# Optimization experiments

Hardware: AMD Instinct MI355X
Metric: run time of the kernel (lower is better)

Reference implementation:

```python
import jax, jax.numpy as jnp
import numpy as np

H = 512      # hidden_size
OUT = 1      # output_size (forced by prev_output shape (B,1,1))
B = 64       # batch
T = 1024     # output_length


def setup_inputs() -> dict:
    key = jax.random.key(0)
    ks = jax.random.split(key, 10)
    s_in = 1.0 / np.sqrt(H)
    return {
        "context_vector": jax.random.normal(ks[0], (B, 1, H), jnp.float32),
        "expected_output": jax.random.normal(ks[1], (B, T, OUT), jnp.float32),
        "W_ih0": jax.random.normal(ks[2], (3 * H, H + OUT), jnp.float32) * s_in,
        "W_hh0": jax.random.normal(ks[3], (3 * H, H), jnp.float32) * s_in,
        "b_ih0": jnp.zeros((3 * H,), jnp.float32),
        "b_hh0": jnp.zeros((3 * H,), jnp.float32),
        "W_ih1": jax.random.normal(ks[4], (3 * H, H), jnp.float32) * s_in,
        "W_hh1": jax.random.normal(ks[5], (3 * H, H), jnp.float32) * s_in,
        "b_ih1": jnp.zeros((3 * H,), jnp.float32),
        "b_hh1": jnp.zeros((3 * H,), jnp.float32),
        "W_o1": jax.random.normal(ks[6], (H, H), jnp.float32) * s_in,
        "b_o1": jnp.zeros((H,), jnp.float32),
        "W_o2": jax.random.normal(ks[7], (OUT, H), jnp.float32) * s_in,
        "b_o2": jnp.zeros((OUT,), jnp.float32),
        "force": 0,  # teacher forcing disabled (original uses python random -> nondeterministic)
    }


def _gru_cell(x, h, W_ih, W_hh, b_ih, b_hh):
    # PyTorch GRU cell math
    gi = x @ W_ih.T + b_ih          # (B, 3H)
    gh = h @ W_hh.T + b_hh          # (B, 3H)
    i_r, i_z, i_n = jnp.split(gi, 3, axis=-1)
    h_r, h_z, h_n = jnp.split(gh, 3, axis=-1)
    r = jax.nn.sigmoid(i_r + h_r)
    z = jax.nn.sigmoid(i_z + h_z)
    n = jnp.tanh(i_n + r * h_n)
    return (1.0 - z) * n + z * h


def reference(context_vector, expected_output, W_ih0, W_hh0, b_ih0, b_hh0,
              W_ih1, W_hh1, b_ih1, b_hh1, W_o1, b_o1, W_o2, b_o2, force):
    del force  # force=False path only (deterministic)
    batch = context_vector.shape[0]
    out_len = expected_output.shape[1]
    ctx = context_vector[:, 0, :]                      # (B, H)
    h0 = jnp.zeros((batch, H), context_vector.dtype)
    h1 = jnp.zeros((batch, H), context_vector.dtype)
    prev = jnp.zeros((batch, OUT), context_vector.dtype)

    def step(carry, _):
        h0, h1, prev = carry
        x = jnp.concatenate([ctx, prev], axis=1)       # (B, H+1)
        h0n = _gru_cell(x, h0, W_ih0, W_hh0, b_ih0, b_hh0)
        h1n = _gru_cell(h0n, h1, W_ih1, W_hh1, b_ih1, b_hh1)
        y = jax.nn.relu(h1n @ W_o1.T + b_o1)           # (B, H)
        y = jax.nn.relu(y @ W_o2.T + b_o2)             # (B, 1)
        return (h0n, h1n, y), y

    (h0, h1, _), ys = jax.lax.scan(step, (h0, h1, prev), None, length=out_len)
    outputs = jnp.transpose(ys, (1, 0, 2))             # (B, T, 1)
    h_i = jnp.stack([h0, h1], axis=0)                  # (n_layers, B, H)
    return outputs, h_i
```

## Files before the change

### kernel.cpp

```cpp
#include <hip/hip_runtime.h>
#include <stdint.h>


#define NWG 256
#define NT  256
#define TT  1024

typedef unsigned short ushort;
typedef unsigned int   uint;
typedef __attribute__((ext_vector_type(8))) short short8;
typedef __attribute__((ext_vector_type(4))) float f32x4;
typedef __attribute__((ext_vector_type(4))) uint  uint4v;

struct __align__(16) SmemR0 {
  ushort wpl[2][48*520];
  float  gictx[3*16*68];
  float  wcol[3][16];
  float  bhnN[16];
  float  prevS[64];
};
struct __align__(16) SmemR2 {
  ushort whh[2][48*520];
  ushort wih[48*520];
  float  xk[3][64][16];
  float  bsumR[16], bsumZ[16], binN[16], bhnN[16];
};
struct __align__(16) SmemR3 {
  ushort wpl[2][16*520];
  float  xk[2][64][4];
  float  bo1v[16], wo2v[16];
};

__device__ __forceinline__ float frcp(float x){
#if __has_builtin(__builtin_amdgcn_rcpf)
  return __builtin_amdgcn_rcpf(x);
#else
  return 1.f/x;
#endif
}
__device__ __forceinline__ float sigm(float x){ return frcp(1.f + __expf(-x)); }
__device__ __forceinline__ float tanh_f(float x){
  return 1.f - 2.f*frcp(__expf(2.f*x) + 1.f);
}
__device__ __forceinline__ float bf2f(ushort h){ return __uint_as_float(((uint)h)<<16); }
__device__ __forceinline__ ushort bfrnd(float x){
  uint u = __float_as_uint(x);
  return (ushort)((u + 0x7fffu + ((u>>16)&1u)) >> 16);
}
#define SWP(p, v)  (void)__hip_atomic_exchange((uint*)(p), (uint)(v), __ATOMIC_RELAXED, __HIP_MEMORY_SCOPE_AGENT)
#define ALD1(p)    __hip_atomic_load((const uint*)(p), __ATOMIC_RELAXED, __HIP_MEMORY_SCOPE_AGENT)
#define ALDF(p)    __uint_as_float(ALD1(p))
#define FADDI(p)   (void)__hip_atomic_fetch_add((p), 1, __ATOMIC_RELAXED, __HIP_MEMORY_SCOPE_AGENT)

__device__ __forceinline__ void gbar(int* slots, int* epoch, int w, int tid, int e){
  __syncthreads();
  if (tid == 0)
    __hip_atomic_store(&slots[w], e, __ATOMIC_RELEASE, __HIP_MEMORY_SCOPE_AGENT);
  if (w == 0 && tid < 64){
    for(;;){
      int m0 = __hip_atomic_load(&slots[tid*4+0], __ATOMIC_RELAXED, __HIP_MEMORY_SCOPE_AGENT);
      int m1 = __hip_atomic_load(&slots[tid*4+1], __ATOMIC_RELAXED, __HIP_MEMORY_SCOPE_AGENT);
      int m2 = __hip_atomic_load(&slots[tid*4+2], __ATOMIC_RELAXED, __HIP_MEMORY_SCOPE_AGENT);
      int m3 = __hip_atomic_load(&slots[tid*4+3], __ATOMIC_RELAXED, __HIP_MEMORY_SCOPE_AGENT);
      if (__all(min(min(m0,m1),min(m2,m3)) >= e)) break;
      __builtin_amdgcn_s_sleep(1);
    }
    if (tid == 0){
      __builtin_amdgcn_fence(__ATOMIC_ACQUIRE, "agent");
      __hip_atomic_store(epoch, e, __ATOMIC_RELEASE, __HIP_MEMORY_SCOPE_AGENT);
    }
  }
  if (tid == 0){
    while (__hip_atomic_load(epoch, __ATOMIC_RELAXED, __HIP_MEMORY_SCOPE_AGENT) < e)
      __builtin_amdgcn_s_sleep(1);
    __builtin_amdgcn_fence(__ATOMIC_ACQUIRE, "agent");
  }
  __syncthreads();
}

__device__ __forceinline__ void drain_sync(){
  __builtin_amdgcn_s_waitcnt(0);
  __syncthreads();
}
__device__ __forceinline__ void waitmail(const int* w, int target, int tid){
  if (tid == 0)
    while ((int)ALD1(w) < target) {}
  __syncthreads();
}
__device__ __forceinline__ void waitmail2(const int* a, const int* b, int target, int tid){
  if (tid == 0)
    while ((int)ALD1(a) < target || (int)ALD1(b) < target) {}
  __syncthreads();
}

#define LD1SCD(dst, addr) \
  asm volatile("global_load_dword %0, %1, off sc0 sc1" : "=v"(dst) : "v"(addr));
#define STSH(addr, val) \
  asm volatile("global_store_short %0, %1, off sc0 sc1" :: "v"(addr), "v"(val) : "memory");
#define ST4SC(addr, val) \
  asm volatile("global_store_dwordx4 %0, %1, off sc0 sc1" :: "v"(addr), "v"(val) : "memory");
#define LD4A(DST, P, OFS) \
  asm volatile("global_load_dwordx4 %0, %1, off sc0 sc1" : "=v"(DST) : "v"((P) + (OFS)));
#define VMBAR4(a,b,c,d) \
  asm volatile("s_waitcnt vmcnt(0)" : "+v"(a),"+v"(b),"+v"(c),"+v"(d));
#define VMBAR8(a,b,c,d,e,f,g,h) \
  asm volatile("s_waitcnt vmcnt(0)" \
               : "+v"(a),"+v"(b),"+v"(c),"+v"(d),"+v"(e),"+v"(f),"+v"(g),"+v"(h));

#define MFMA_ __builtin_amdgcn_mfma_f32_16x16x32_bf16

#define DECL_HILO(PH, PL) \
  uint4v ha0,ha1,ha2,ha3,ha4,ha5,ha6,ha7,ha8,ha9,ha10,ha11,ha12,ha13,ha14,ha15; \
  uint4v la0,la1,la2,la3,la4,la5,la6,la7,la8,la9,la10,la11,la12,la13,la14,la15; \
  LD4A(ha0,PH,aoffB+0*32) LD4A(ha1,PH,aoffB+1*32) LD4A(ha2,PH,aoffB+2*32) LD4A(ha3,PH,aoffB+3*32) \
  LD4A(ha4,PH,aoffB+4*32) LD4A(ha5,PH,aoffB+5*32) LD4A(ha6,PH,aoffB+6*32) LD4A(ha7,PH,aoffB+7*32) \
  LD4A(ha8,PH,aoffB+8*32) LD4A(ha9,PH,aoffB+9*32) LD4A(ha10,PH,aoffB+10*32) LD4A(ha11,PH,aoffB+11*32) \
  LD4A(ha12,PH,aoffB+12*32) LD4A(ha13,PH,aoffB+13*32) LD4A(ha14,PH,aoffB+14*32) LD4A(ha15,PH,aoffB+15*32) \
  LD4A(la0,PL,aoffB+0*32) LD4A(la1,PL,aoffB+1*32) LD4A(la2,PL,aoffB+2*32) LD4A(la3,PL,aoffB+3*32) \
  LD4A(la4,PL,aoffB+4*32) LD4A(la5,PL,aoffB+5*32) LD4A(la6,PL,aoffB+6*32) LD4A(la7,PL,aoffB+7*32) \
  LD4A(la8,PL,aoffB+8*32) LD4A(la9,PL,aoffB+9*32) LD4A(la10,PL,aoffB+10*32) LD4A(la11,PL,aoffB+11*32) \
  LD4A(la12,PL,aoffB+12*32) LD4A(la13,PL,aoffB+13*32) LD4A(la14,PL,aoffB+14*32) LD4A(la15,PL,aoffB+15*32) \
  VMBAR8(ha0,ha1,ha2,ha3,ha4,ha5,ha6,ha7) \
  VMBAR8(ha8,ha9,ha10,ha11,ha12,ha13,ha14,ha15) \
  VMBAR8(la0,la1,la2,la3,la4,la5,la6,la7) \
  VMBAR8(la8,la9,la10,la11,la12,la13,la14,la15)

#define MS3F(i) { \
  short8 AH_ = __builtin_bit_cast(short8, ha##i); \
  short8 AL_ = __builtin_bit_cast(short8, la##i); \
  const int ko_ = (i)*32 + q*8; \
  short8 bh_ = *(const short8*)(&S0.wpl[0][(col)*520 + ko_]); \
  short8 bl_ = *(const short8*)(&S0.wpl[1][(col)*520 + ko_]); \
  acc0 = MFMA_(AH_, bh_, acc0, 0,0,0); \
  acc0 = MFMA_(AL_, bh_, acc0, 0,0,0); \
  acc0 = MFMA_(AH_, bl_, acc0, 0,0,0); \
  bh_ = *(const short8*)(&S0.wpl[0][(16+col)*520 + ko_]); \
  bl_ = *(const short8*)(&S0.wpl[1][(16+col)*520 + ko_]); \
  acc1 = MFMA_(AH_, bh_, acc1, 0,0,0); \
  acc1 = MFMA_(AL_, bh_, acc1, 0,0,0); \
  acc1 = MFMA_(AH_, bl_, acc1, 0,0,0); \
  bh_ = *(const short8*)(&S0.wpl[0][(32+col)*520 + ko_]); \
  bl_ = *(const short8*)(&S0.wpl[1][(32+col)*520 + ko_]); \
  acc2 = MFMA_(AH_, bh_, acc2, 0,0,0); \
  acc2 = MFMA_(AL_, bh_, acc2, 0,0,0); \
  acc2 = MFMA_(AH_, bl_, acc2, 0,0,0); }

#define GH1(i) { \
  short8 AH_ = __builtin_bit_cast(short8, ha##i); \
  short8 AL_ = __builtin_bit_cast(short8, la##i); \
  const int ko_ = kq + (i)*32 + q*8; \
  short8 bh_ = *(const short8*)(&S2.whh[0][(col)*520 + ko_]); \
  short8 bl_ = *(const short8*)(&S2.whh[1][(col)*520 + ko_]); \
  aR = MFMA_(AH_, bh_, aR, 0,0,0); \
  aR = MFMA_(AL_, bh_, aR, 0,0,0); \
  aR = MFMA_(AH_, bl_, aR, 0,0,0); \
  bh_ = *(const short8*)(&S2.whh[0][(16+col)*520 + ko_]); \
  bl_ = *(const short8*)(&S2.whh[1][(16+col)*520 + ko_]); \
  aZ = MFMA_(AH_, bh_, aZ, 0,0,0); \
  aZ = MFMA_(AL_, bh_, aZ, 0,0,0); \
  aZ = MFMA_(AH_, bl_, aZ, 0,0,0); \
  bh_ = *(const short8*)(&S2.whh[0][(32+col)*520 + ko_]); \
  bl_ = *(const short8*)(&S2.whh[1][(32+col)*520 + ko_]); \
  aNh = MFMA_(AH_, bh_, aNh, 0,0,0); \
  aNh = MFMA_(AL_, bh_, aNh, 0,0,0); \
  aNh = MFMA_(AH_, bl_, aNh, 0,0,0); }

#define GI1(i) { \
  short8 AH_ = __builtin_bit_cast(short8, ga##i); \
  const int ko_ = kq + (i)*32 + q*8; \
  short8 bh_ = *(const short8*)(&S2.wih[(col)*520 + ko_]); \
  aR = MFMA_(AH_, bh_, aR, 0,0,0); \
  bh_ = *(const short8*)(&S2.wih[(16+col)*520 + ko_]); \
  aZ = MFMA_(AH_, bh_, aZ, 0,0,0); \
  bh_ = *(const short8*)(&S2.wih[(32+col)*520 + ko_]); \
  aNi = MFMA_(AH_, bh_, aNi, 0,0,0); }

#define DECL_HI8(P) \
  uint4v ha0,ha1,ha2,ha3,ha4,ha5,ha6,ha7; \
  LD4A(ha0,P,aoff8+0*32) LD4A(ha1,P,aoff8+1*32) LD4A(ha2,P,aoff8+2*32) LD4A(ha3,P,aoff8+3*32) \
  LD4A(ha4,P,aoff8+4*32) LD4A(ha5,P,aoff8+5*32) LD4A(ha6,P,aoff8+6*32) LD4A(ha7,P,aoff8+7*32) \
  VMBAR8(ha0,ha1,ha2,ha3,ha4,ha5,ha6,ha7)

#define MS1H(i) { \
  short8 AH_ = __builtin_bit_cast(short8, ha##i); \
  const int ko_ = kb + (i)*32 + q*8; \
  short8 bh_ = *(const short8*)(&S3.wpl[0][(col)*520 + ko_]); \
  short8 bl_ = *(const short8*)(&S3.wpl[1][(col)*520 + ko_]); \
  acc0 = MFMA_(AH_, bh_, acc0, 0,0,0); \
  acc0 = MFMA_(AH_, bl_, acc0, 0,0,0); }

#define RUN16(M) M(0) M(1) M(2) M(3) M(4) M(5) M(6) M(7) \
                 M(8) M(9) M(10) M(11) M(12) M(13) M(14) M(15)
#define RUN8(M)  M(0) M(1) M(2) M(3) M(4) M(5) M(6) M(7)
#define RUN4(M)  M(0) M(1) M(2) M(3)

extern "C" __global__ void __launch_bounds__(NT, 1)
decoder_rnn(const float* __restrict__ ctx,
            const float* __restrict__ Wih0,
            const float* __restrict__ Whh0,
            const float* __restrict__ bih0,
            const float* __restrict__ bhh0g,
            const float* __restrict__ Wih1,
            const float* __restrict__ Whh1,
            const float* __restrict__ bih1g,
            const float* __restrict__ bhh1g,
            const float* __restrict__ Wo1,
            const float* __restrict__ bo1g,
            const float* __restrict__ Wo2,
            const float* __restrict__ bo2g,
            float* __restrict__ out,
            float* __restrict__ ws)
{
  extern __shared__ char smem_raw[];
  SmemR0& S0 = *reinterpret_cast<SmemR0*>(smem_raw);
  SmemR2& S2 = *reinterpret_cast<SmemR2*>(smem_raw);
  SmemR3& S3 = *reinterpret_cast<SmemR3*>(smem_raw);
  const int tid = threadIdx.x;
  const int wg  = blockIdx.x;

  ushort* hp  = (ushort*)ws;
  float* yout = (float*)ws + 196608;
  int*  ibase = (int*)((float*)ws + 200704);
  int* gslots = ibase;
  int* epoch  = ibase + 256;
  int* mbox   = ibase + 512;

  const float bo2v = bo2g[0];

  for (int i = wg*NT + tid; i < 200704; i += NWG*NT)
    SWP((uint*)ws + i, 0u);
  if (wg == 0)
    for (int i = tid; i < 256*32; i += NT) SWP(mbox + i, 0);

  const int gid   = wg >> 7;
  const int m     = wg & 127;
  const int bbase = 32*gid;
  int role, j, bh = 0;
  if (m < 32){ role = 0; j = m; }
  else if (m < 96){ role = 2; bh = (m - 32) >> 5; j = m & 31; }
  else { role = 3; j = m - 96; }

  if (role == 0){
    for (int i = tid; i < 48*512; i += NT){
      int r = i >> 9, k = i & 511;
      int g3 = r >> 4, n = r & 15;
      float wv = Whh0[(size_t)(g3*512 + 16*j + n)*512 + k];
      ushort hh = bfrnd(wv);
      S0.wpl[0][r*520 + k] = hh;
      S0.wpl[1][r*520 + k] = bfrnd(wv - bf2f(hh));
    }
    if (tid < 48){
      int g3 = tid >> 4, n = tid & 15;
      S0.wcol[g3][n] = Wih0[(size_t)(g3*512 + 16*j + n)*513 + 512];
    }
    if (tid < 16) S0.bhnN[tid] = bhh0g[2*512 + 16*j + tid];
    for (int idx = tid; idx < 1536; idx += NT){
      int r = idx >> 5, bl = idx & 31;
      int g3 = r >> 4, n = r & 15;
      int grow = g3*512 + 16*j + n;
      const float* wr = Wih0 + (size_t)grow*513;
      const float* cx = ctx  + (size_t)(bbase + bl)*512;
      float s = bih0[grow];
      if (g3 < 2) s += bhh0g[grow];
      #pragma unroll 4
      for (int k = 0; k < 512; ++k) s += wr[k]*cx[k];
      S0.gictx[g3*1088 + n*68 + bl] = s;
    }
  } else if (role == 2){
    for (int i = tid; i < 48*512; i += NT){
      int r = i >> 9, k = i & 511;
      int g3 = r >> 4, n = r & 15;
      size_t row = (size_t)(g3*512 + 16*j + n)*512 + k;
      float wv = Whh1[row];
      ushort hh = bfrnd(wv);
      S2.whh[0][r*520 + k] = hh;
      S2.whh[1][r*520 + k] = bfrnd(wv - bf2f(hh));
      S2.wih[r*520 + k] = bfrnd(Wih1[row]);
    }
    if (tid < 16){
      int n = tid;
      S2.bsumR[n] = bih1g[16*j + n]       + bhh1g[16*j + n];
      S2.bsumZ[n] = bih1g[512 + 16*j + n] + bhh1g[512 + 16*j + n];
      S2.binN[n]  = bih1g[1024 + 16*j + n];
      S2.bhnN[n]  = bhh1g[1024 + 16*j + n];
    }
  } else {
    for (int i = tid; i < 16*512; i += NT){
      int r = i >> 9, k = i & 511;
      float wv = Wo1[(size_t)(16*j + r)*512 + k];
      ushort hh = bfrnd(wv);
      S3.wpl[0][r*520 + k] = hh;
      S3.wpl[1][r*520 + k] = bfrnd(wv - bf2f(hh));
    }
    if (tid < 16){ S3.bo1v[tid] = bo1g[16*j + tid]; S3.wo2v[tid] = Wo2[16*j + tid]; }
  }

  gbar(gslots, epoch, wg, tid, 1);

  int* myline = mbox + wg*32;
  const int gb = gid*128;

  const int v   = tid >> 6;
  const int l   = tid & 63;
  const int q   = l >> 4;
  const int col = l & 15;
  const int ng  = 16*j + col;

  if (role == 0){
    const int bblk  = v & 1;
    const int aoffB = (bbase + 16*bblk + col)*512 + q*8;
    const int b0wL  = 16*bblk + 4*q;
    float hc0 = 0.f, hc1 = 0.f, hc2 = 0.f, hc3 = 0.f;
    for (int t = 0; t < TT; ++t){
      const int r0 = t & 1, w0 = r0 ^ 1;
      waitmail(myline + 0, 32*t, tid);
      const ushort* rH = hp + r0*32768;
      const ushort* rL = hp + 65536 + r0*32768;
      ushort*       wH = hp + w0*32768;
      ushort*       wL = hp + 65536 + w0*32768;
      f32x4 acc0={0,0,0,0}, acc1={0,0,0,0}, acc2={0,0,0,0};
      if (v < 2){
        DECL_HILO(rH, rL)
        RUN16(MS3F)
      }
      waitmail(myline + 1, 32*t, tid);
      if (tid < 32){
        float s = 0.f;
        if (t > 0){
          const float* yp = yout + ((t-1)&1)*2048 + bbase + tid;
          float vv[32];
          #pragma unroll
          for (int jj = 0; jj < 32; ++jj)
            LD1SCD(vv[jj], yp + jj*64)
          VMBAR8(vv[0],vv[1],vv[2],vv[3],vv[4],vv[5],vv[6],vv[7])
          VMBAR8(vv[8],vv[9],vv[10],vv[11],vv[12],vv[13],vv[14],vv[15])
          VMBAR8(vv[16],vv[17],vv[18],vv[19],vv[20],vv[21],vv[22],vv[23])
          VMBAR8(vv[24],vv[25],vv[26],vv[27],vv[28],vv[29],vv[30],vv[31])
          #pragma unroll
          for (int jj = 0; jj < 32; ++jj) s += vv[jj];
        }
        float pv = fmaxf(s + bo2v, 0.f);
        S0.prevS[tid] = pv;
        if (j == 0 && t > 0) out[(size_t)(bbase + tid)*TT + (t-1)] = pv;
      }
      __syncthreads();
      if (v < 2){
        f32x4 pv4 = *(const f32x4*)&S0.prevS[b0wL];
        f32x4 gR = *(const f32x4*)&S0.gictx[0*1088 + col*68 + b0wL];
        f32x4 gZ = *(const f32x4*)&S0.gictx[1*1088 + col*68 + b0wL];
        f32x4 gN = *(const f32x4*)&S0.gictx[2*1088 + col*68 + b0wL];
        float wc0 = S0.wcol[0][col], wc1 = S0.wcol[1][col], wc2 = S0.wcol[2][col];
        float bhn = S0.bhnN[col];
        #define E0(i, HC) { \
          float rr = sigm(gR[i] + pv4[i]*wc0 + acc0[i]); \
          float zz = sigm(gZ[i] + pv4[i]*wc1 + acc1[i]); \
          float nn = tanh_f(gN[i] + pv4[i]*wc2 + rr*(acc2[i] + bhn)); \
          float h = (1.f-zz)*nn + zz*HC; \
          HC = h; \
          ushort hh_ = bfrnd(h); \
          uint hu_ = hh_, lu_ = bfrnd(h - bf2f(hh_)); \
          STSH(wH + (size_t)(bbase + b0wL + (i))*512 + ng, hu_) \
          STSH(wL + (size_t)(bbase + b0wL + (i))*512 + ng, lu_) }
        E0(0,hc0) E0(1,hc1) E0(2,hc2) E0(3,hc3)
        #undef E0
      }
      drain_sync();
      if (tid < 96)
        FADDI(mbox + (gb + tid)*32 + 0);
    }
  } else if (role == 2){
    ushort* p1H = hp + 131072;
    ushort* p1L = hp + 163840;
    const int bb16  = bbase + 16*bh;
    const int kq    = v*128;
    const int aoffA = (bb16 + col)*512 + kq + q*8;
    float hc0 = 0.f, hc1 = 0.f, hc2 = 0.f, hc3 = 0.f;
    for (int t = 0; t < TT; ++t){
      const int w0 = (t & 1) ^ 1;
      waitmail(myline + 1 + bh, 32*t, tid);
      f32x4 aR={0,0,0,0}, aZ={0,0,0,0}, aNi={0,0,0,0}, aNh={0,0,0,0};
      {
        uint4v ha0,ha1,ha2,ha3, la0,la1,la2,la3;
        LD4A(ha0, p1H, aoffA+0*32) LD4A(ha1, p1H, aoffA+1*32)
        LD4A(ha2, p1H, aoffA+2*32) LD4A(ha3, p1H, aoffA+3*32)
        LD4A(la0, p1L, aoffA+0*32) LD4A(la1, p1L, aoffA+1*32)
        LD4A(la2, p1L, aoffA+2*32) LD4A(la3, p1L, aoffA+3*32)
        VMBAR8(ha0,ha1,ha2,ha3,la0,la1,la2,la3)
        RUN4(GH1)
      }
      waitmail(myline + 0, 32*(t+1), tid);
      {
        const ushort* rH = hp + w0*32768;
        uint4v ga0,ga1,ga2,ga3;
        LD4A(ga0, rH, aoffA+0*32) LD4A(ga1, rH, aoffA+1*32)
        LD4A(ga2, rH, aoffA+2*32) LD4A(ga3, rH, aoffA+3*32)
        VMBAR4(ga0,ga1,ga2,ga3)
        RUN4(GI1)
      }
      if (v >= 1){
        *(f32x4*)&S2.xk[v-1][l][0]  = aR;
        *(f32x4*)&S2.xk[v-1][l][4]  = aZ;
        *(f32x4*)&S2.xk[v-1][l][8]  = aNi;
        *(f32x4*)&S2.xk[v-1][l][12] = aNh;
      }
      __syncthreads();
      if (v == 0){
        #pragma unroll
        for (int w = 0; w < 3; ++w){
          aR  += *(const f32x4*)&S2.xk[w][l][0];
          aZ  += *(const f32x4*)&S2.xk[w][l][4];
          aNi += *(const f32x4*)&S2.xk[w][l][8];
          aNh += *(const f32x4*)&S2.xk[w][l][12];
        }
        float bsR = S2.bsumR[col], bsZ = S2.bsumZ[col];
        float biN = S2.binN[col],  bhN = S2.bhnN[col];
        #define E1(i, HC) { \
          float r1 = sigm(aR[i] + bsR); \
          float z1 = sigm(aZ[i] + bsZ); \
          float n1 = tanh_f(aNi[i] + biN + r1*(aNh[i] + bhN)); \
          float h = (1.f-z1)*n1 + z1*HC; \
          HC = h; \
          ushort hh_ = bfrnd(h); \
          uint hu_ = hh_, lu_ = bfrnd(h - bf2f(hh_)); \
          STSH(p1H + (size_t)(bb16 + 4*q + (i))*512 + ng, hu_) \
          STSH(p1L + (size_t)(bb16 + 4*q + (i))*512 + ng, lu_) }
        E1(0,hc0) E1(1,hc1) E1(2,hc2) E1(3,hc3)
        #undef E1
      }
      drain_sync();
      if (tid < 96)
        FADDI(mbox + (gb + 32 + tid)*32 + 1 + bh);
    }
  } else {
    const ushort* rH = hp + 131072;
    const int bblk  = v & 1;
    const int kb    = (v >> 1)*256;
    const int aoff8 = (bbase + 16*bblk + col)*512 + kb + q*8;
    const int b0wL  = 16*bblk + 4*q;
    for (int t = 0; t < TT; ++t){
      waitmail2(myline + 1, myline + 2, 32*(t+1), tid);
      f32x4 acc0={0,0,0,0};
      {
        DECL_HI8(rH)
        RUN8(MS1H)
      }
      if (v >= 2)
        *(f32x4*)&S3.xk[bblk][l][0] = acc0;
      __syncthreads();
      if (v < 2){
        acc0 += *(const f32x4*)&S3.xk[bblk][l][0];
        float s0 = S3.wo2v[col]*fmaxf(acc0[0] + S3.bo1v[col], 0.f);
        float s1 = S3.wo2v[col]*fmaxf(acc0[1] + S3.bo1v[col], 0.f);
        float s2 = S3.wo2v[col]*fmaxf(acc0[2] + S3.bo1v[col], 0.f);
        float s3 = S3.wo2v[col]*fmaxf(acc0[3] + S3.bo1v[col], 0.f);
        #pragma unroll
        for (int d = 1; d < 16; d <<= 1){
          s0 += __shfl_xor(s0, d);
          s1 += __shfl_xor(s1, d);
          s2 += __shfl_xor(s2, d);
          s3 += __shfl_xor(s3, d);
        }
        if (col == 0){
          float* rp = yout + (t&1)*2048 + j*64 + bbase + b0wL;
          f32x4 sv = {s0, s1, s2, s3};
          ST4SC(rp, sv)
        }
      }
      drain_sync();
      if (tid < 32)
        FADDI(mbox + (gb + tid)*32 + 1);
    }
  }

  gbar(gslots, epoch, wg, tid, 2);
  if (wg == 0 && tid < 64){
    float s = 0.f;
    const float* yp = yout + 2048 + tid;
    #pragma unroll
    for (int jj = 0; jj < 32; ++jj) s += ALDF(yp + jj*64);
    out[(size_t)tid*TT + 1023] = fmaxf(s + bo2v, 0.f);
  }
  {
    int g = wg*256 + tid;
    if (g < 32768) out[65536 + g] = bf2f(hp[g]) + bf2f(hp[65536 + g]);
    else {
      int g2 = g - 32768;
      out[65536 + g] = bf2f(hp[131072 + g2]) + bf2f(hp[163840 + g2]);
    }
  }
}

extern "C" void kernel_launch(void* const* d_in, const int* in_sizes, int n_in,
                              void* d_out, int out_size, void* d_ws, size_t ws_size,
                              hipStream_t stream){
  const float* ctx   = (const float*)d_in[0];
  const float* Wih0  = (const float*)d_in[2];
  const float* Whh0  = (const float*)d_in[3];
  const float* bih0  = (const float*)d_in[4];
  const float* bhh0  = (const float*)d_in[5];
  const float* Wih1  = (const float*)d_in[6];
  const float* Whh1  = (const float*)d_in[7];
  const float* bih1  = (const float*)d_in[8];
  const float* bhh1  = (const float*)d_in[9];
  const float* Wo1   = (const float*)d_in[10];
  const float* bo1   = (const float*)d_in[11];
  const float* Wo2   = (const float*)d_in[12];
  const float* bo2   = (const float*)d_in[13];

  (void)in_sizes; (void)n_in; (void)out_size; (void)ws_size;

  const int smem_sz = (int)sizeof(SmemR2);
  (void)hipFuncSetAttribute((const void*)decoder_rnn,
                            hipFuncAttributeMaxDynamicSharedMemorySize,
                            smem_sz);

  decoder_rnn<<<NWG, NT, smem_sz, stream>>>(
      ctx, Wih0, Whh0, bih0, bhh0, Wih1, Whh1, bih1, bhh1,
      Wo1, bo1, Wo2, bo2, (float*)d_out, (float*)d_ws);
}
```

Before: 8.770 ms.

## Replace atomic-counter mailboxes with per-producer flag slots polled as vector loads

Each producer workgroup now writes its step number into its own dword slot in a wider mailbox line, instead of atomically incrementing a shared counter. Consumers poll the whole 32-slot line with eight dwordx4 loads and take the minimum. The aim is to avoid contention from many fetch_add atomics hitting the same address on every timestep. The mailbox area triples in size, and polling now issues more load traffic per iteration. The prev-output sum also changes from a serial loop to a tree reduction.

```diff
diff --git a/kernel.cpp b/kernel.cpp
--- a/kernel.cpp
+++ b/kernel.cpp
@@ -50,7 +50,6 @@
 #define SWP(p, v)  (void)__hip_atomic_exchange((uint*)(p), (uint)(v), __ATOMIC_RELAXED, __HIP_MEMORY_SCOPE_AGENT)
 #define ALD1(p)    __hip_atomic_load((const uint*)(p), __ATOMIC_RELAXED, __HIP_MEMORY_SCOPE_AGENT)
 #define ALDF(p)    __uint_as_float(ALD1(p))
-#define FADDI(p)   (void)__hip_atomic_fetch_add((p), 1, __ATOMIC_RELAXED, __HIP_MEMORY_SCOPE_AGENT)
 
 __device__ __forceinline__ void gbar(int* slots, int* epoch, int w, int tid, int e){
   __syncthreads();
@@ -82,21 +81,13 @@
   __builtin_amdgcn_s_waitcnt(0);
   __syncthreads();
 }
-__device__ __forceinline__ void waitmail(const int* w, int target, int tid){
-  if (tid == 0)
-    while ((int)ALD1(w) < target) {}
-  __syncthreads();
-}
-__device__ __forceinline__ void waitmail2(const int* a, const int* b, int target, int tid){
-  if (tid == 0)
-    while ((int)ALD1(a) < target || (int)ALD1(b) < target) {}
-  __syncthreads();
-}
 
 #define LD1SCD(dst, addr) \
   asm volatile("global_load_dword %0, %1, off sc0 sc1" : "=v"(dst) : "v"(addr));
 #define STSH(addr, val) \
   asm volatile("global_store_short %0, %1, off sc0 sc1" :: "v"(addr), "v"(val) : "memory");
+#define STI(addr, val) \
+  asm volatile("global_store_dword %0, %1, off sc0 sc1" :: "v"(addr), "v"(val) : "memory");
 #define ST4SC(addr, val) \
   asm volatile("global_store_dwordx4 %0, %1, off sc0 sc1" :: "v"(addr), "v"(val) : "memory");
 #define LD4A(DST, P, OFS) \
@@ -106,6 +97,47 @@
 #define VMBAR8(a,b,c,d,e,f,g,h) \
   asm volatile("s_waitcnt vmcnt(0)" \
                : "+v"(a),"+v"(b),"+v"(c),"+v"(d),"+v"(e),"+v"(f),"+v"(g),"+v"(h));
+
+__device__ __forceinline__ int min4i(uint4v a){
+  return min(min((int)a.x,(int)a.y), min((int)a.z,(int)a.w));
+}
+__device__ __forceinline__ void waitline(const int* line, int target, int tid){
+  if (tid == 0){
+    const uint* p = (const uint*)line;
+    for(;;){
+      uint4v a0,a1,a2,a3,a4,a5,a6,a7;
+      LD4A(a0,p,0)  LD4A(a1,p,4)  LD4A(a2,p,8)  LD4A(a3,p,12)
+      LD4A(a4,p,16) LD4A(a5,p,20) LD4A(a6,p,24) LD4A(a7,p,28)
+      VMBAR8(a0,a1,a2,a3,a4,a5,a6,a7)
+      int m = min(min(min(min4i(a0),min4i(a1)),min(min4i(a2),min4i(a3))),
+                  min(min(min4i(a4),min4i(a5)),min(min4i(a6),min4i(a7))));
+      if (m >= target) break;
+    }
+  }
+  __syncthreads();
+}
+__device__ __forceinline__ void waitline2(const int* la, const int* lb, int target, int tid){
+  if (tid == 0){
+    const uint* pa = (const uint*)la;
+    const uint* pb = (const uint*)lb;
+    for(;;){
+      uint4v a0,a1,a2,a3,a4,a5,a6,a7;
+      uint4v b0,b1,b2,b3,b4,b5,b6,b7;
+      LD4A(a0,pa,0)  LD4A(a1,pa,4)  LD4A(a2,pa,8)  LD4A(a3,pa,12)
+      LD4A(a4,pa,16) LD4A(a5,pa,20) LD4A(a6,pa,24) LD4A(a7,pa,28)
+      LD4A(b0,pb,0)  LD4A(b1,pb,4)  LD4A(b2,pb,8)  LD4A(b3,pb,12)
+      LD4A(b4,pb,16) LD4A(b5,pb,20) LD4A(b6,pb,24) LD4A(b7,pb,28)
+      VMBAR8(a0,a1,a2,a3,a4,a5,a6,a7)
+      VMBAR8(b0,b1,b2,b3,b4,b5,b6,b7)
+      int ma = min(min(min(min4i(a0),min4i(a1)),min(min4i(a2),min4i(a3))),
+                   min(min(min4i(a4),min4i(a5)),min(min4i(a6),min4i(a7))));
+      int mb = min(min(min(min4i(b0),min4i(b1)),min(min4i(b2),min4i(b3))),
+                   min(min(min4i(b4),min4i(b5)),min(min4i(b6),min4i(b7))));
+      if (min(ma,mb) >= target) break;
+    }
+  }
+  __syncthreads();
+}
 
 #define MFMA_ __builtin_amdgcn_mfma_f32_16x16x32_bf16
 
@@ -230,7 +262,7 @@
   for (int i = wg*NT + tid; i < 200704; i += NWG*NT)
     SWP((uint*)ws + i, 0u);
   if (wg == 0)
-    for (int i = tid; i < 256*32; i += NT) SWP(mbox + i, 0);
+    for (int i = tid; i < 256*96; i += NT) SWP(mbox + i, 0);
 
   const int gid   = wg >> 7;
   const int m     = wg & 127;
@@ -297,7 +329,7 @@
 
   gbar(gslots, epoch, wg, tid, 1);
 
-  int* myline = mbox + wg*32;
+  int* myline = mbox + wg*96;
   const int gb = gid*128;
 
   const int v   = tid >> 6;
@@ -313,7 +345,7 @@
     float hc0 = 0.f, hc1 = 0.f, hc2 = 0.f, hc3 = 0.f;
     for (int t = 0; t < TT; ++t){
       const int r0 = t & 1, w0 = r0 ^ 1;
-      waitmail(myline + 0, 32*t, tid);
+      waitline(myline + 0, t, tid);
       const ushort* rH = hp + r0*32768;
       const ushort* rL = hp + 65536 + r0*32768;
       ushort*       wH = hp + w0*32768;
@@ -323,7 +355,7 @@
         DECL_HILO(rH, rL)
         RUN16(MS3F)
       }
-      waitmail(myline + 1, 32*t, tid);
+      waitline(myline + 32, t, tid);
       if (tid < 32){
         float s = 0.f;
         if (t > 0){
@@ -337,7 +369,9 @@
           VMBAR8(vv[16],vv[17],vv[18],vv[19],vv[20],vv[21],vv[22],vv[23])
           VMBAR8(vv[24],vv[25],vv[26],vv[27],vv[28],vv[29],vv[30],vv[31])
           #pragma unroll
-          for (int jj = 0; jj < 32; ++jj) s += vv[jj];
+          for (int st = 16; st >= 1; st >>= 1)
+            for (int k2 = 0; k2 < st; ++k2) vv[k2] += vv[k2 + st];
+          s = vv[0];
         }
         float pv = fmaxf(s + bo2v, 0.f);
         S0.prevS[tid] = pv;
@@ -366,7 +400,7 @@
       }
       drain_sync();
       if (tid < 96)
-        FADDI(mbox + (gb + tid)*32 + 0);
+        STI(mbox + (gb + tid)*96 + j, t + 1)
     }
   } else if (role == 2){
     ushort* p1H = hp + 131072;
@@ -377,7 +411,7 @@
     float hc0 = 0.f, hc1 = 0.f, hc2 = 0.f, hc3 = 0.f;
     for (int t = 0; t < TT; ++t){
       const int w0 = (t & 1) ^ 1;
-      waitmail(myline + 1 + bh, 32*t, tid);
+      waitline(myline + 32*(1 + bh), t, tid);
       f32x4 aR={0,0,0,0}, aZ={0,0,0,0}, aNi={0,0,0,0}, aNh={0,0,0,0};
       {
         uint4v ha0,ha1,ha2,ha3, la0,la1,la2,la3;
@@ -388,7 +422,7 @@
         VMBAR8(ha0,ha1,ha2,ha3,la0,la1,la2,la3)
         RUN4(GH1)
       }
-      waitmail(myline + 0, 32*(t+1), tid);
+      waitline(myline + 0, t + 1, tid);
       {
         const ushort* rH = hp + w0*32768;
         uint4v ga0,ga1,ga2,ga3;
@@ -429,7 +463,7 @@
       }
       drain_sync();
       if (tid < 96)
-        FADDI(mbox + (gb + 32 + tid)*32 + 1 + bh);
+        STI(mbox + (gb + 32 + tid)*96 + 32*(1 + bh) + j, t + 1)
     }
   } else {
     const ushort* rH = hp + 131072;
@@ -438,7 +472,7 @@
     const int aoff8 = (bbase + 16*bblk + col)*512 + kb + q*8;
     const int b0wL  = 16*bblk + 4*q;
     for (int t = 0; t < TT; ++t){
-      waitmail2(myline + 1, myline + 2, 32*(t+1), tid);
+      waitline2(myline + 32, myline + 64, t + 1, tid);
       f32x4 acc0={0,0,0,0};
       {
         DECL_HI8(rH)
@@ -468,7 +502,7 @@
       }
       drain_sync();
       if (tid < 32)
-        FADDI(mbox + (gb + tid)*32 + 1);
+        STI(mbox + (gb + tid)*96 + 32 + j, t + 1)
     }
   }
 
```

Measured after the change: 10.55 ms. 1.2x slower.

## Tag payload LSBs with phase bits so consumers validate data instead of draining stores

Applied to the files above, without the earlier changes.

The hidden-state and y-output stores now carry a phase tag in their least-significant bit, and every consumer spins, re-loading until all loaded words carry the expected tag. This lets each producer replace the per-step store drain (drain_sync) with a plain __syncthreads before posting its mailbox increment, which removes the wait for store completion from the critical path of the recurrence. In exchange it gives up one mantissa bit of each bf16 hi/lo half and of the fp32 partial outputs, and it adds retry loops with sleep. It also relies on mailbox/data reordering being caught by the tag check.

```diff
diff --git a/kernel.cpp b/kernel.cpp
--- a/kernel.cpp
+++ b/kernel.cpp
@@ -106,6 +106,14 @@
 #define VMBAR8(a,b,c,d,e,f,g,h) \
   asm volatile("s_waitcnt vmcnt(0)" \
                : "+v"(a),"+v"(b),"+v"(c),"+v"(d),"+v"(e),"+v"(f),"+v"(g),"+v"(h));
+
+#define TAGM 0x00010001u
+#define FOLDV(V) fo_ |= ((V.x^em_)&TAGM)|((V.y^em_)&TAGM)| \
+                        ((V.z^em_)&TAGM)|((V.w^em_)&TAGM);
+#define FOLD4(p)  FOLDV(p##0) FOLDV(p##1) FOLDV(p##2) FOLDV(p##3)
+#define FOLD8(p)  FOLD4(p) FOLDV(p##4) FOLDV(p##5) FOLDV(p##6) FOLDV(p##7)
+#define FOLD16(p) FOLD8(p) FOLDV(p##8) FOLDV(p##9) FOLDV(p##10) FOLDV(p##11) \
+                  FOLDV(p##12) FOLDV(p##13) FOLDV(p##14) FOLDV(p##15)
 
 #define MFMA_ __builtin_amdgcn_mfma_f32_16x16x32_bf16
 
@@ -320,31 +328,57 @@
       ushort*       wL = hp + 65536 + w0*32768;
       f32x4 acc0={0,0,0,0}, acc1={0,0,0,0}, acc2={0,0,0,0};
       if (v < 2){
-        DECL_HILO(rH, rL)
-        RUN16(MS3F)
+        const uint em_ = (t==0) ? 0u : (((((t-1)>>1)&1u)^1u) * TAGM);
+        for(;;){
+          DECL_HILO(rH, rL)
+          uint fo_ = 0u;
+          FOLD16(ha) FOLD16(la)
+          if (__all((int)(fo_ == 0u))){ RUN16(MS3F) break; }
+          __builtin_amdgcn_s_sleep(1);
+        }
       }
       waitmail(myline + 1, 32*t, tid);
-      if (tid < 32){
+      if (v == 0){
         float s = 0.f;
         if (t > 0){
-          const float* yp = yout + ((t-1)&1)*2048 + bbase + tid;
-          float vv[32];
-          #pragma unroll
-          for (int jj = 0; jj < 32; ++jj)
-            LD1SCD(vv[jj], yp + jj*64)
-          VMBAR8(vv[0],vv[1],vv[2],vv[3],vv[4],vv[5],vv[6],vv[7])
-          VMBAR8(vv[8],vv[9],vv[10],vv[11],vv[12],vv[13],vv[14],vv[15])
-          VMBAR8(vv[16],vv[17],vv[18],vv[19],vv[20],vv[21],vv[22],vv[23])
-          VMBAR8(vv[24],vv[25],vv[26],vv[27],vv[28],vv[29],vv[30],vv[31])
-          #pragma unroll
-          for (int jj = 0; jj < 32; ++jj) s += vv[jj];
-        }
-        float pv = fmaxf(s + bo2v, 0.f);
-        S0.prevS[tid] = pv;
-        if (j == 0 && t > 0) out[(size_t)(bbase + tid)*TT + (t-1)] = pv;
+          const uint ey_ = (((t-1)>>1)&1u)^1u;
+          const float* yp = yout + ((t-1)&1)*2048 + bbase + l;
+          for(;;){
+            float vv[32]; uint fo_ = 0u;
+            if (l < 32){
+              #pragma unroll
+              for (int jj = 0; jj < 32; ++jj)
+                LD1SCD(vv[jj], yp + jj*64)
+              VMBAR8(vv[0],vv[1],vv[2],vv[3],vv[4],vv[5],vv[6],vv[7])
+              VMBAR8(vv[8],vv[9],vv[10],vv[11],vv[12],vv[13],vv[14],vv[15])
+              VMBAR8(vv[16],vv[17],vv[18],vv[19],vv[20],vv[21],vv[22],vv[23])
+              VMBAR8(vv[24],vv[25],vv[26],vv[27],vv[28],vv[29],vv[30],vv[31])
+              #pragma unroll
+              for (int jj = 0; jj < 32; ++jj)
+                fo_ |= (__float_as_uint(vv[jj]) ^ ey_) & 1u;
+            }
+            if (__all((int)(fo_ == 0u))){
+              if (l < 32){
+                #pragma unroll
+                for (int st = 16; st >= 1; st >>= 1)
+                  #pragma unroll
+                  for (int k2 = 0; k2 < st; ++k2) vv[k2] += vv[k2 + st];
+                s = vv[0];
+              }
+              break;
+            }
+            __builtin_amdgcn_s_sleep(1);
+          }
+        }
+        if (l < 32){
+          float pv = fmaxf(s + bo2v, 0.f);
+          S0.prevS[l] = pv;
+          if (j == 0 && t > 0) out[(size_t)(bbase + l)*TT + (t-1)] = pv;
+        }
       }
       __syncthreads();
       if (v < 2){
+        const uint tg0_ = ((t>>1)&1u)^1u;
         f32x4 pv4 = *(const f32x4*)&S0.prevS[b0wL];
         f32x4 gR = *(const f32x4*)&S0.gictx[0*1088 + col*68 + b0wL];
         f32x4 gZ = *(const f32x4*)&S0.gictx[1*1088 + col*68 + b0wL];
@@ -357,14 +391,14 @@
           float nn = tanh_f(gN[i] + pv4[i]*wc2 + rr*(acc2[i] + bhn)); \
           float h = (1.f-zz)*nn + zz*HC; \
           HC = h; \
-          ushort hh_ = bfrnd(h); \
-          uint hu_ = hh_, lu_ = bfrnd(h - bf2f(hh_)); \
+          uint hu_ = ((uint)bfrnd(h) & 0xFFFEu) | tg0_; \
+          uint lu_ = ((uint)bfrnd(h - bf2f((ushort)hu_)) & 0xFFFEu) | tg0_; \
           STSH(wH + (size_t)(bbase + b0wL + (i))*512 + ng, hu_) \
           STSH(wL + (size_t)(bbase + b0wL + (i))*512 + ng, lu_) }
         E0(0,hc0) E0(1,hc1) E0(2,hc2) E0(3,hc3)
         #undef E0
       }
-      drain_sync();
+      __syncthreads();
       if (tid < 96)
         FADDI(mbox + (gb + tid)*32 + 0);
     }
@@ -376,26 +410,37 @@
     const int aoffA = (bb16 + col)*512 + kq + q*8;
     float hc0 = 0.f, hc1 = 0.f, hc2 = 0.f, hc3 = 0.f;
     for (int t = 0; t < TT; ++t){
-      const int w0 = (t & 1) ^ 1;
       waitmail(myline + 1 + bh, 32*t, tid);
       f32x4 aR={0,0,0,0}, aZ={0,0,0,0}, aNi={0,0,0,0}, aNh={0,0,0,0};
       {
-        uint4v ha0,ha1,ha2,ha3, la0,la1,la2,la3;
-        LD4A(ha0, p1H, aoffA+0*32) LD4A(ha1, p1H, aoffA+1*32)
-        LD4A(ha2, p1H, aoffA+2*32) LD4A(ha3, p1H, aoffA+3*32)
-        LD4A(la0, p1L, aoffA+0*32) LD4A(la1, p1L, aoffA+1*32)
-        LD4A(la2, p1L, aoffA+2*32) LD4A(la3, p1L, aoffA+3*32)
-        VMBAR8(ha0,ha1,ha2,ha3,la0,la1,la2,la3)
-        RUN4(GH1)
+        const uint em_ = (t==0) ? 0u : ((((t-1)&1u)^1u) * TAGM);
+        for(;;){
+          uint4v ha0,ha1,ha2,ha3, la0,la1,la2,la3;
+          LD4A(ha0, p1H, aoffA+0*32) LD4A(ha1, p1H, aoffA+1*32)
+          LD4A(ha2, p1H, aoffA+2*32) LD4A(ha3, p1H, aoffA+3*32)
+          LD4A(la0, p1L, aoffA+0*32) LD4A(la1, p1L, aoffA+1*32)
+          LD4A(la2, p1L, aoffA+2*32) LD4A(la3, p1L, aoffA+3*32)
+          VMBAR8(ha0,ha1,ha2,ha3,la0,la1,la2,la3)
+          uint fo_ = 0u;
+          FOLD4(ha) FOLD4(la)
+          if (__all((int)(fo_ == 0u))){ RUN4(GH1) break; }
+          __builtin_amdgcn_s_sleep(1);
+        }
       }
       waitmail(myline + 0, 32*(t+1), tid);
       {
-        const ushort* rH = hp + w0*32768;
-        uint4v ga0,ga1,ga2,ga3;
-        LD4A(ga0, rH, aoffA+0*32) LD4A(ga1, rH, aoffA+1*32)
-        LD4A(ga2, rH, aoffA+2*32) LD4A(ga3, rH, aoffA+3*32)
-        VMBAR4(ga0,ga1,ga2,ga3)
-        RUN4(GI1)
+        const uint em_ = (((t>>1)&1u)^1u) * TAGM;
+        const ushort* rH = hp + ((t & 1) ^ 1)*32768;
+        for(;;){
+          uint4v ga0,ga1,ga2,ga3;
+          LD4A(ga0, rH, aoffA+0*32) LD4A(ga1, rH, aoffA+1*32)
+          LD4A(ga2, rH, aoffA+2*32) LD4A(ga3, rH, aoffA+3*32)
+          VMBAR4(ga0,ga1,ga2,ga3)
+          uint fo_ = 0u;
+          FOLD4(ga)
+          if (__all((int)(fo_ == 0u))){ RUN4(GI1) break; }
+          __builtin_amdgcn_s_sleep(1);
+        }
       }
       if (v >= 1){
         *(f32x4*)&S2.xk[v-1][l][0]  = aR;
@@ -405,6 +450,7 @@
       }
       __syncthreads();
       if (v == 0){
+        const uint tg1_ = (t&1u)^1u;
         #pragma unroll
         for (int w = 0; w < 3; ++w){
           aR  += *(const f32x4*)&S2.xk[w][l][0];
@@ -420,14 +466,14 @@
           float n1 = tanh_f(aNi[i] + biN + r1*(aNh[i] + bhN)); \
           float h = (1.f-z1)*n1 + z1*HC; \
           HC = h; \
-          ushort hh_ = bfrnd(h); \
-          uint hu_ = hh_, lu_ = bfrnd(h - bf2f(hh_)); \
+          uint hu_ = ((uint)bfrnd(h) & 0xFFFEu) | tg1_; \
+          uint lu_ = ((uint)bfrnd(h - bf2f((ushort)hu_)) & 0xFFFEu) | tg1_; \
           STSH(p1H + (size_t)(bb16 + 4*q + (i))*512 + ng, hu_) \
           STSH(p1L + (size_t)(bb16 + 4*q + (i))*512 + ng, lu_) }
         E1(0,hc0) E1(1,hc1) E1(2,hc2) E1(3,hc3)
         #undef E1
       }
-      drain_sync();
+      __syncthreads();
       if (tid < 96)
         FADDI(mbox + (gb + 32 + tid)*32 + 1 + bh);
     }
@@ -441,8 +487,14 @@
       waitmail2(myline + 1, myline + 2, 32*(t+1), tid);
       f32x4 acc0={0,0,0,0};
       {
-        DECL_HI8(rH)
-        RUN8(MS1H)
+        const uint em_ = ((t&1u)^1u) * TAGM;
+        for(;;){
+          DECL_HI8(rH)
+          uint fo_ = 0u;
+          FOLD8(ha)
+          if (__all((int)(fo_ == 0u))){ RUN8(MS1H) break; }
+          __builtin_amdgcn_s_sleep(1);
+        }
       }
       if (v >= 2)
         *(f32x4*)&S3.xk[bblk][l][0] = acc0;
@@ -461,17 +513,22 @@
           s3 += __shfl_xor(s3, d);
         }
         if (col == 0){
-          float* rp = yout + (t&1)*2048 + j*64 + bbase + b0wL;
-          f32x4 sv = {s0, s1, s2, s3};
-          ST4SC(rp, sv)
-        }
-      }
-      drain_sync();
+          const uint tgy_ = ((t>>1)&1u)^1u;
+          uint* rp = (uint*)(yout + (t&1)*2048 + j*64 + bbase + b0wL);
+          uint4v uv = { (__float_as_uint(s0) & ~1u) | tgy_,
+                        (__float_as_uint(s1) & ~1u) | tgy_,
+                        (__float_as_uint(s2) & ~1u) | tgy_,
+                        (__float_as_uint(s3) & ~1u) | tgy_ };
+          ST4SC(rp, uv)
+        }
+      }
+      __syncthreads();
       if (tid < 32)
         FADDI(mbox + (gb + tid)*32 + 1);
     }
   }
 
+  drain_sync();
   gbar(gslots, epoch, wg, tid, 2);
   if (wg == 0 && tid < 64){
     float s = 0.f;
```

Result: faster. 8.451 ms (-3.6%).
